# Kernel tuning notes

Measured on AMD Instinct MI355X. Metric: run time of the kernel, lower is better.

Reference implementation:

```python
import jax, jax.numpy as jnp
import numpy as np

N = 32768      # nodes
E = 524288     # edges (avg degree 16)
F = 64         # node_feat_dim
D = 64         # gnn_dim (= per-head out channels, concat=False)
ED = 32        # edge_feat_dim
L = 6          # num_layers
H = 2          # heads
C = D          # per-head channels
LN_EPS = 1e-5


def layer_norm(h, g, b):
    mu = jnp.mean(h, axis=-1, keepdims=True)
    var = jnp.mean((h - mu) ** 2, axis=-1, keepdims=True)
    return g * (h - mu) * jax.lax.rsqrt(var + LN_EPS) + b


def setup_inputs() -> dict:
    key = jax.random.key(0)
    ks = jax.random.split(key, 16)
    x = jax.random.normal(ks[0], (N, F), jnp.float32)
    edge_index = jax.random.randint(ks[1], (2, E), 0, N, jnp.int32)
    edge_attr = jax.random.normal(ks[2], (E, ED), jnp.float32)
    manual_gamma = 1.0 + 0.1 * jax.random.normal(ks[3], (L, D), jnp.float32)
    manual_beta = 0.1 * jax.random.normal(ks[4], (L, D), jnp.float32)
    # node_embed Linear(F, D)
    embed_W = jax.random.normal(ks[5], (F, D), jnp.float32) / np.float32(np.sqrt(F))
    embed_b = jnp.zeros((D,), jnp.float32)
    # per-layer LayerNorm affine params
    ln_gamma = jnp.ones((L, D), jnp.float32)
    ln_beta = jnp.zeros((L, D), jnp.float32)
    # per-layer GATConv params (shared lin for src/dst, PyG non-bipartite)
    lin_W = jax.random.normal(ks[6], (L, D, H * C), jnp.float32) / np.float32(np.sqrt(D))
    lin_edge_W = jax.random.normal(ks[7], (L, ED, H * C), jnp.float32) / np.float32(np.sqrt(ED))
    att_src = jax.random.normal(ks[8], (L, H, C), jnp.float32) / np.float32(np.sqrt(C))
    att_dst = jax.random.normal(ks[9], (L, H, C), jnp.float32) / np.float32(np.sqrt(C))
    att_edge = jax.random.normal(ks[10], (L, H, C), jnp.float32) / np.float32(np.sqrt(C))
    gat_bias = jnp.zeros((L, C), jnp.float32)
    # edge output head: Linear(2D+ED, D) -> ReLU -> Linear(D, 1)
    head_W1 = jax.random.normal(ks[11], (2 * D + ED, D), jnp.float32) / np.float32(np.sqrt(2 * D + ED))
    head_b1 = jnp.zeros((D,), jnp.float32)
    head_W2 = jax.random.normal(ks[12], (D, 1), jnp.float32) / np.float32(np.sqrt(D))
    head_b2 = jnp.zeros((1,), jnp.float32)
    return dict(x=x, edge_index=edge_index, edge_attr=edge_attr,
                manual_gamma=manual_gamma, manual_beta=manual_beta,
                embed_W=embed_W, embed_b=embed_b, ln_gamma=ln_gamma, ln_beta=ln_beta,
                lin_W=lin_W, lin_edge_W=lin_edge_W, att_src=att_src, att_dst=att_dst,
                att_edge=att_edge, gat_bias=gat_bias, head_W1=head_W1, head_b1=head_b1,
                head_W2=head_W2, head_b2=head_b2)


def reference(x, edge_index, edge_attr, manual_gamma, manual_beta,
              embed_W, embed_b, ln_gamma, ln_beta, lin_W, lin_edge_W,
              att_src, att_dst, att_edge, gat_bias, head_W1, head_b1,
              head_W2, head_b2):
    src, dst = edge_index[0], edge_index[1]
    # PyG GATConv default add_self_loops=True, fill_value='mean' for edge_attr
    loop = jnp.arange(N, dtype=edge_index.dtype)
    src_f = jnp.concatenate([src, loop])   # [E+N]
    dst_f = jnp.concatenate([dst, loop])
    deg = jax.ops.segment_sum(jnp.ones((E,), x.dtype), dst, num_segments=N)
    loop_attr = jax.ops.segment_sum(edge_attr, dst, num_segments=N) / jnp.maximum(deg, 1.0)[:, None]
    edge_attr_f = jnp.concatenate([edge_attr, loop_attr], axis=0)  # [E+N, ED]

    h = x @ embed_W + embed_b  # [N, D]
    for l in range(L):
        hn = layer_norm(h, ln_gamma[l], ln_beta[l])
        hm = manual_gamma[l][None, :] * hn + manual_beta[l][None, :]
        xh = (hm @ lin_W[l]).reshape(N, H, C)                      # [N,H,C]
        a_s = jnp.sum(xh * att_src[l][None], axis=-1)              # [N,H]
        a_d = jnp.sum(xh * att_dst[l][None], axis=-1)              # [N,H]
        eh = (edge_attr_f @ lin_edge_W[l]).reshape(-1, H, C)       # [E+N,H,C]
        a_e = jnp.sum(eh * att_edge[l][None], axis=-1)             # [E+N,H]
        alpha = jax.nn.leaky_relu(a_s[src_f] + a_d[dst_f] + a_e, 0.2)
        amax = jax.ops.segment_max(alpha, dst_f, num_segments=N)   # every node has a self-loop
        ex = jnp.exp(alpha - amax[dst_f])
        den = jax.ops.segment_sum(ex, dst_f, num_segments=N)
        w = ex / (den[dst_f] + 1e-16)                              # segment softmax [E+N,H]
        msg = xh[src_f] * w[..., None]                             # [E+N,H,C]
        out = jax.ops.segment_sum(msg, dst_f, num_segments=N)      # [N,H,C]
        h = jax.nn.relu(jnp.mean(out, axis=1) + gat_bias[l])       # concat=False -> head mean

    ef = jnp.concatenate([h[src], h[dst], edge_attr], axis=-1)     # [E, 2D+ED]
    hid = jax.nn.relu(ef @ head_W1 + head_b1)
    return (hid @ head_W2 + head_b2)[:, 0]                         # [E]
```

## Files before the change

### kernel.cpp

```cpp
#include <hip/hip_runtime.h>
#include <hip/hip_bf16.h>
#include <math.h>

#define NN 32768
#define EE 524288
#define LL 6

typedef __attribute__((ext_vector_type(8))) short short8;
typedef __attribute__((ext_vector_type(4))) float floatx4;
typedef __attribute__((ext_vector_type(4))) float fx4;
typedef __attribute__((ext_vector_type(4))) unsigned int ux4;

union U16x8 { short8 v; unsigned short u[8]; };

__device__ __forceinline__ unsigned short f2bf(float x) {
    union { float f; unsigned int u; } v; v.f = x;
    unsigned int r = v.u + 0x7fffu + ((v.u >> 16) & 1u);
    return (unsigned short)(r >> 16);
}
__device__ __forceinline__ float bf2f(unsigned short h) {
    union { unsigned int u; float f; } v; v.u = (unsigned int)h << 16;
    return v.f;
}


__global__ __launch_bounds__(1024) void scan_kernel(const int* __restrict__ deg,
                                                    int* __restrict__ row_ptr,
                                                    int* __restrict__ cnt) {
    __shared__ int bs[1024];
    int t = threadIdx.x;
    int base = t * 32;
    int loc[32];
    int s = 0;
#pragma unroll
    for (int i = 0; i < 32; ++i) { int v = deg[base + i]; loc[i] = s; s += v; }
    bs[t] = s;
    __syncthreads();
    for (int off = 1; off < 1024; off <<= 1) {
        int v = (t >= off) ? bs[t - off] : 0;
        __syncthreads();
        bs[t] += v;
        __syncthreads();
    }
    int pre = (t == 0) ? 0 : bs[t - 1];
#pragma unroll
    for (int i = 0; i < 32; ++i) { row_ptr[base + i] = pre + loc[i]; cnt[base + i] = 0; }
    if (t == 1023) row_ptr[NN] = bs[1023];
}

__global__ void fill_kernel(const int* __restrict__ src, const int* __restrict__ dst,
                            const float* __restrict__ aeo, const int* __restrict__ row_ptr,
                            int* __restrict__ cnt, float* __restrict__ aeP) {
    int e = blockIdx.x * 256 + threadIdx.x;
    if (e >= EE) return;
    int d = dst[e];
    int pos = row_ptr[d] + atomicAdd(&cnt[d], 1);
    const float2* ae2 = (const float2*)aeo;
    float2 a0 = ae2[e],          a1 = ae2[EE + e],     a2 = ae2[2 * EE + e];
    float2 a3 = ae2[3 * EE + e], a4 = ae2[4 * EE + e], a5 = ae2[5 * EE + e];
    fx4 r0 = {__int_as_float(src[e]), 0.f, a0.x, a0.y};
    fx4 r1 = {a1.x, a1.y, a2.x, a2.y};
    fx4 r2 = {a3.x, a3.y, a4.x, a4.y};
    fx4 r3 = {a5.x, a5.y, 0.f, 0.f};
    fx4* R = (fx4*)(aeP + (size_t)pos * 16);
    R[0] = r0; R[1] = r1; R[2] = r2; R[3] = r3;
}

__global__ __launch_bounds__(256) void smallprep_kernel(
    const float* __restrict__ lin_W, const float* __restrict__ head_W1,
    const float* __restrict__ lin_edge_W, const float* __restrict__ att_edge,
    const float* __restrict__ att_src, const float* __restrict__ att_dst,
    unsigned short* __restrict__ gBhi, unsigned short* __restrict__ gBlo,
    unsigned short* __restrict__ aeBhi, unsigned short* __restrict__ aeBlo,
    float* __restrict__ vs, float* __restrict__ vvd,
    unsigned short* __restrict__ w1chi, unsigned short* __restrict__ w1clo,
    int* __restrict__ deg) {
    __shared__ float svb[384];
    int bb = blockIdx.x;
    int tid = threadIdx.x;
    if (bb < 7) {
        unsigned short* dh = gBhi + (size_t)bb * 128 * 64;
        unsigned short* dl = gBlo + (size_t)bb * 128 * 64;
        if (bb < 6) {
            int n2 = tid & 63, kh = tid >> 6;
            U16x8 hh[4], ll[4];
            for (int kk = 0; kk < 32; ++kk) {
                int j = kh * 32 + kk;
                int h = j >> 6, k = j & 63;
                float wv = 0.5f * lin_W[((size_t)bb * 64 + k) * 128 + h * 64 + n2];
                unsigned short h16 = f2bf(wv);
                hh[kk >> 3].u[kk & 7] = h16;
                ll[kk >> 3].u[kk & 7] = f2bf(wv - bf2f(h16));
            }
#pragma unroll
            for (int c = 0; c < 4; ++c) {
                int cg = kh * 4 + c;
                int off = n2 * 128 + ((cg ^ (n2 & 15)) << 3);
                *(short8*)(dh + off) = hh[c].v;
                *(short8*)(dl + off) = ll[c].v;
            }
        } else {
            int n = tid & 127, kh = tid >> 7;
            U16x8 hh[4], ll[4];
            for (int kk = 0; kk < 32; ++kk) {
                int k = kh * 32 + kk;
                float wv = (n < 64) ? head_W1[k * 64 + n] : head_W1[(64 + k) * 64 + (n - 64)];
                unsigned short h16 = f2bf(wv);
                hh[kk >> 3].u[kk & 7] = h16;
                ll[kk >> 3].u[kk & 7] = f2bf(wv - bf2f(h16));
            }
#pragma unroll
            for (int c = 0; c < 4; ++c) {
                int cg = kh * 4 + c;
                int off = n * 64 + ((cg ^ (n & 7)) << 3);
                *(short8*)(dh + off) = hh[c].v;
                *(short8*)(dl + off) = ll[c].v;
            }
        }
    } else if (bb == 7) {
        for (int t = tid; t < 384; t += 256) {
            int l = t / 64; int r = t & 63; int ed = r >> 1; int hh = r & 1;
            const float* w = lin_edge_W + l * 32 * 128 + ed * 128 + hh * 64;
            const float* a = att_edge + l * 128 + hh * 64;
            float s = 0.f;
#pragma unroll 8
            for (int c = 0; c < 64; ++c) s += w[c] * a[c];
            svb[t] = s;
        }
        int n = tid & 63, kc = tid >> 6;
#pragma unroll
        for (int j = 0; j < 8; ++j) {
            int k = kc * 8 + j;
            float wv = head_W1[(128 + k) * 64 + n];
            unsigned short h16 = f2bf(wv);
            w1chi[n * 32 + k] = h16;
            w1clo[n * 32 + k] = f2bf(wv - bf2f(h16));
        }
        __syncthreads();
        if (tid < 64) {
            int n2 = tid & 15, q = tid >> 4;
            U16x8 hi, lo;
#pragma unroll
            for (int i = 0; i < 8; ++i) {
                int k = q * 8 + i;
                float val = (n2 < 12) ? svb[(n2 >> 1) * 64 + k * 2 + (n2 & 1)] : 0.f;
                unsigned short h16 = f2bf(val);
                hi.u[i] = h16;
                lo.u[i] = f2bf(val - bf2f(h16));
            }
            *(short8*)(aeBhi + tid * 8) = hi.v;
            *(short8*)(aeBlo + tid * 8) = lo.v;
        }
    } else if (bb < 14) {
        int l = bb - 8;
        int sel = tid >> 7, idx = tid & 127;
        int h = idx >> 6, k = idx & 63;
        const float* att = (sel ? att_dst : att_src) + l * 128 + h * 64;
        const float* wr = lin_W + ((size_t)l * 64 + k) * 128 + h * 64;
        float s = 0.f;
#pragma unroll 8
        for (int c = 0; c < 64; ++c) s += wr[c] * att[c];
        (sel ? vvd : vs)[l * 128 + idx] = s;
    } else {
        int i = (bb - 14) * 1024 + tid * 4;
        *(int4*)(deg + i) = make_int4(0, 0, 0, 0);
    }
}

__global__ __launch_bounds__(256) void ae_deg_kernel(
    const float* __restrict__ edge_attr, const int* __restrict__ dst,
    const unsigned short* __restrict__ aeBhi, const unsigned short* __restrict__ aeBlo,
    float* __restrict__ aeo, unsigned short* __restrict__ eabf, int* __restrict__ deg) {
    __shared__ float tr[4][64 * 13];
    int tid = threadIdx.x;
    int w = tid >> 6, lane = tid & 63;
    int e0 = blockIdx.x * 256 + w * 64;
    int e = blockIdx.x * 256 + tid;
    atomicAdd(&deg[dst[e]], 1);
    short8 bhi = *(const short8*)(aeBhi + lane * 8);
    short8 blo = *(const short8*)(aeBlo + lane * 8);
    int r = lane & 15, q = lane >> 4;
    float* trw = tr[w];
#pragma unroll
    for (int t = 0; t < 4; ++t) {
        int er = e0 + t * 16 + r;
        const fx4* p = (const fx4*)(edge_attr + (size_t)er * 32 + q * 8);
        fx4 f0 = __builtin_nontemporal_load(p);
        fx4 f1 = __builtin_nontemporal_load(p + 1);
        float av[8] = {f0.x, f0.y, f0.z, f0.w, f1.x, f1.y, f1.z, f1.w};
        U16x8 hi, lo;
#pragma unroll
        for (int jj = 0; jj < 8; ++jj) {
            unsigned short h16 = f2bf(av[jj]);
            hi.u[jj] = h16;
            lo.u[jj] = f2bf(av[jj] - bf2f(h16));
        }
        __builtin_nontemporal_store(hi.v, (short8*)(eabf + (size_t)er * 32 + q * 8));
        floatx4 acc = {};
        acc = __builtin_amdgcn_mfma_f32_16x16x32_bf16(lo.v, bhi, acc, 0, 0, 0);
        acc = __builtin_amdgcn_mfma_f32_16x16x32_bf16(hi.v, blo, acc, 0, 0, 0);
        acc = __builtin_amdgcn_mfma_f32_16x16x32_bf16(hi.v, bhi, acc, 0, 0, 0);
        if (r < 12) {
#pragma unroll
            for (int rr = 0; rr < 4; ++rr)
                trw[(t * 16 + q * 4 + rr) * 13 + r] = acc[rr];
        }
    }
#pragma unroll
    for (int l = 0; l < LL; ++l) {
        float2 v2;
        v2.x = trw[lane * 13 + l * 2];
        v2.y = trw[lane * 13 + l * 2 + 1];
        *(float2*)(aeo + (size_t)l * EE * 2 + (size_t)(e0 + lane) * 2) = v2;
    }
}

__global__ __launch_bounds__(256) void embed_ln_kernel(
    const float* __restrict__ x, const float* __restrict__ W, const float* __restrict__ b,
    const float* __restrict__ ln_g, const float* __restrict__ ln_b,
    const float* __restrict__ mg, const float* __restrict__ mb,
    const float* __restrict__ vs0, const float* __restrict__ vd0,
    unsigned short* __restrict__ hm_bf, float* __restrict__ a_s, float* __restrict__ a_d) {
    __shared__ float xr[4][64];
    int w = threadIdx.x >> 6, j = threadIdx.x & 63;
    int n = blockIdx.x * 4 + w;
    xr[w][j] = x[(size_t)n * 64 + j];
    __syncthreads();
    float acc = b[j];
#pragma unroll 8
    for (int k = 0; k < 64; ++k) acc += xr[w][k] * W[k * 64 + j];
    float s = acc, sq = acc * acc;
    for (int off = 1; off < 64; off <<= 1) { s += __shfl_xor(s, off); sq += __shfl_xor(sq, off); }
    float mu = s * (1.f / 64.f);
    float var = sq * (1.f / 64.f) - mu * mu;
    float rs = rsqrtf(var + 1e-5f);
    float hm = mg[j] * (ln_g[j] * (acc - mu) * rs + ln_b[j]) + mb[j];
    hm_bf[(size_t)n * 64 + j] = f2bf(hm);
    float s0 = hm * vs0[j], s1 = hm * vs0[64 + j];
    float d0 = hm * vd0[j], d1 = hm * vd0[64 + j];
    for (int off = 1; off < 64; off <<= 1) {
        s0 += __shfl_xor(s0, off); s1 += __shfl_xor(s1, off);
        d0 += __shfl_xor(d0, off); d1 += __shfl_xor(d1, off);
    }
    if (j == 0) {
        a_s[n * 2] = s0; a_s[n * 2 + 1] = s1;
        a_d[n * 2] = d0; a_d[n * 2 + 1] = d1;
    }
}

__device__ __forceinline__ void fma8h(uint4 pv, float w, float* a) {
    unsigned int u[4] = {pv.x, pv.y, pv.z, pv.w};
#pragma unroll
    for (int q = 0; q < 4; ++q) {
        union { unsigned int x; float f; } lo, hi;
        lo.x = u[q] << 16; hi.x = u[q] & 0xffff0000u;
        a[2 * q]     += w * lo.f;
        a[2 * q + 1] += w * hi.f;
    }
}

__global__ __launch_bounds__(256) void aggregate10_kernel(
    const unsigned short* __restrict__ hm_bf, const float* __restrict__ a_s,
    const float* __restrict__ a_d, const float* __restrict__ aeP,
    const int* __restrict__ row_ptr, unsigned short* __restrict__ Abf, int aeoff) {
    __shared__ float stg[4][4][64][4];
    int w = threadIdx.x >> 6, lane = threadIdx.x & 63;
    int g = lane >> 4, j = lane & 15;
    int ch = j & 7, hh = j >> 3;
    int n = blockIdx.x * 16 + w * 4 + g;
    const float2* as2 = (const float2*)a_s;
    const uint4* hmv = (const uint4*)hm_bf;
    float2 adn = ((const float2*)a_d)[n];
    float2 asn = as2[n];
    uint4 pvself = hmv[(size_t)n * 8 + ch];
    int beg = row_ptr[n], end = row_ptr[n + 1];
    int degn = end - beg;

    float acc[8] = {};
    float den = 0.f, aex = 0.f, aey = 0.f;
    float* sg = &stg[w][g][0][0];

    for (int base = 0; base < degn; base += 64) {
        int cnt = degn - base; cnt = cnt > 64 ? 64 : cnt;
        int nchunk = (cnt + 15) >> 4;
        for (int it = 0; it < nchunk; ++it) {
            int s0 = it * 16;
            int rem = cnt - s0;
            float w0v = 0.f, w1v = 0.f;
            int sval = 0;
            if (j < rem) {
                const char* rec = (const char*)aeP + ((size_t)(beg + base + s0 + j) << 6);
                int sv = *(const int*)rec;
                float2 ae = *(const float2*)(rec + aeoff);
                float2 as = as2[sv];
                aex += ae.x; aey += ae.y;
                float al0 = as.x + adn.x + ae.x; al0 = al0 > 0.f ? al0 : 0.2f * al0;
                float al1 = as.y + adn.y + ae.y; al1 = al1 > 0.f ? al1 : 0.2f * al1;
                w0v = __expf(al0);
                w1v = __expf(al1);
                sval = sv;
            }
            float4 st;
            st.x = __int_as_float(sval); st.y = w0v; st.z = w1v; st.w = 0.f;
            *(float4*)(sg + (s0 + j) * 4) = st;
        }
        int c8 = (cnt + 7) & ~7;
        for (int s = 0; s < c8; s += 8) {
            float4 m[8];
#pragma unroll
            for (int u = 0; u < 8; ++u) m[u] = *(const float4*)(sg + (s + u) * 4);
            uint4 p[8];
#pragma unroll
            for (int u = 0; u < 8; ++u) p[u] = hmv[(size_t)__float_as_int(m[u].x) * 8 + ch];
#pragma unroll
            for (int u = 0; u < 8; ++u) {
                float b = hh ? m[u].z : m[u].y;
                den += b;
                fma8h(p[u], b, acc);
            }
        }
    }
#pragma unroll
    for (int m = 1; m < 16; m <<= 1) {
        aex += __shfl_xor(aex, m);
        aey += __shfl_xor(aey, m);
    }
    float invd = 1.f / fmaxf((float)degn, 1.f);
    float al0 = asn.x + adn.x + aex * invd; al0 = al0 > 0.f ? al0 : 0.2f * al0;
    float al1 = asn.y + adn.y + aey * invd; al1 = al1 > 0.f ? al1 : 0.2f * al1;
    float ws = hh ? __expf(al1) : __expf(al0);
    den += ws;
    fma8h(pvself, ws, acc);
    float inv = 1.f / (den + 1e-16f);
    U16x8 hb;
#pragma unroll
    for (int q = 0; q < 8; ++q) hb.u[q] = f2bf(acc[q] * inv);
    int cg = hh * 8 + ch;
    __builtin_nontemporal_store(hb.v, (short8*)(Abf + (size_t)n * 128 + ((cg ^ (n & 15)) << 3)));
}

__global__ __launch_bounds__(256) void post_gemm(
    const unsigned short* __restrict__ Abf, const unsigned short* __restrict__ gBhi,
    const unsigned short* __restrict__ gBlo, const float* __restrict__ bias,
    const float* __restrict__ ln_g, const float* __restrict__ ln_b,
    const float* __restrict__ mg, const float* __restrict__ mb,
    const float* __restrict__ vsn, const float* __restrict__ vdn,
    unsigned short* __restrict__ hm_bf, float* __restrict__ a_s, float* __restrict__ a_d) {
    __shared__ unsigned short Ahi[64 * 128];
    __shared__ unsigned short Bhi[64 * 128], Blo[64 * 128];
    int tid = threadIdx.x;
    {
        const ux4* sa = (const ux4*)(Abf + (size_t)blockIdx.x * 64 * 128);
        const uint4* sh = (const uint4*)gBhi;
        const uint4* sl = (const uint4*)gBlo;
        for (int i = tid; i < 1024; i += 256) {
            ((ux4*)Ahi)[i] = __builtin_nontemporal_load(sa + i);
            ((uint4*)Bhi)[i] = sh[i];
            ((uint4*)Blo)[i] = sl[i];
        }
    }
    __syncthreads();

    int w = tid >> 6, lane = tid & 63, col = lane & 15, quad = lane >> 4;
    int m = w * 16 + col;
    floatx4 acc[4] = {};
#pragma unroll
    for (int s = 0; s < 4; ++s) {
        int ca = (quad + 4 * s) ^ col;
        short8 ahi = *(const short8*)(Ahi + m * 128 + ca * 8);
#pragma unroll
        for (int t = 0; t < 4; ++t) {
            int off = (t * 16 + col) * 128 + ca * 8;
            short8 bhi = *(const short8*)(Bhi + off);
            short8 blo = *(const short8*)(Blo + off);
            acc[t] = __builtin_amdgcn_mfma_f32_16x16x32_bf16(ahi, blo, acc[t], 0, 0, 0);
            acc[t] = __builtin_amdgcn_mfma_f32_16x16x32_bf16(ahi, bhi, acc[t], 0, 0, 0);
        }
    }
    int nodebase = blockIdx.x * 64 + w * 16;
    float bv[4];
#pragma unroll
    for (int t = 0; t < 4; ++t) bv[t] = bias[t * 16 + col];
    float vsv[4], vsv1[4], vdv[4], vdv1[4], lg[4], lb[4], mgv[4], mbv[4];
#pragma unroll
    for (int t = 0; t < 4; ++t) {
        int c = t * 16 + col;
        vsv[t] = vsn[c]; vsv1[t] = vsn[64 + c];
        vdv[t] = vdn[c]; vdv1[t] = vdn[64 + c];
        lg[t] = ln_g[c]; lb[t] = ln_b[c];
        mgv[t] = mg[c]; mbv[t] = mb[c];
    }
#pragma unroll
    for (int r = 0; r < 4; ++r) {
        int node = nodebase + quad * 4 + r;
        float hv[4];
        float s = 0.f, sq = 0.f;
#pragma unroll
        for (int t = 0; t < 4; ++t) {
            float v = acc[t][r] + bv[t];
            v = v > 0.f ? v : 0.f;
            hv[t] = v;
            s += v; sq += v * v;
        }
        for (int off = 1; off < 16; off <<= 1) { s += __shfl_xor(s, off); sq += __shfl_xor(sq, off); }
        float mu = s * (1.f / 64.f);
        float var = sq * (1.f / 64.f) - mu * mu;
        float rs = rsqrtf(var + 1e-5f);
        float s0 = 0.f, s1 = 0.f, d0 = 0.f, d1 = 0.f;
#pragma unroll
        for (int t = 0; t < 4; ++t) {
            float hmv = mgv[t] * (lg[t] * (hv[t] - mu) * rs + lb[t]) + mbv[t];
            hm_bf[(size_t)node * 64 + t * 16 + col] = f2bf(hmv);
            s0 += hmv * vsv[t]; s1 += hmv * vsv1[t];
            d0 += hmv * vdv[t]; d1 += hmv * vdv1[t];
        }
        for (int off = 1; off < 16; off <<= 1) {
            s0 += __shfl_xor(s0, off); s1 += __shfl_xor(s1, off);
            d0 += __shfl_xor(d0, off); d1 += __shfl_xor(d1, off);
        }
        if (col == 0) {
            a_s[node * 2] = s0; a_s[node * 2 + 1] = s1;
            a_d[node * 2] = d0; a_d[node * 2 + 1] = d1;
        }
    }
}

__global__ __launch_bounds__(256) void postuv_gemm(
    const unsigned short* __restrict__ Abf, const unsigned short* __restrict__ gB5hi,
    const unsigned short* __restrict__ gB5lo, const float* __restrict__ bias,
    const unsigned short* __restrict__ gB6hi, const unsigned short* __restrict__ gB6lo,
    unsigned short* __restrict__ uv) {
    __shared__ unsigned short lds[24576];
    unsigned short* Ahi  = lds;
    unsigned short* B5hi = lds + 8192;
    unsigned short* B5lo = lds + 16384;
    unsigned short* A2hi = lds;
    unsigned short* A2lo = lds + 4096;
    unsigned short* B6hi = lds + 8192;
    unsigned short* B6lo = lds + 16384;
    int tid = threadIdx.x;
    {
        const ux4* sa = (const ux4*)(Abf + (size_t)blockIdx.x * 64 * 128);
        const uint4* sh = (const uint4*)gB5hi;
        const uint4* sl = (const uint4*)gB5lo;
        for (int i = tid; i < 1024; i += 256) {
            ((ux4*)Ahi)[i] = __builtin_nontemporal_load(sa + i);
            ((uint4*)B5hi)[i] = sh[i];
            ((uint4*)B5lo)[i] = sl[i];
        }
    }
    __syncthreads();

    int w = tid >> 6, lane = tid & 63, col = lane & 15, quad = lane >> 4;
    int m = w * 16 + col;
    floatx4 acc[4] = {};
#pragma unroll
    for (int s = 0; s < 4; ++s) {
        int ca = (quad + 4 * s) ^ col;
        short8 ahi = *(const short8*)(Ahi + m * 128 + ca * 8);
#pragma unroll
        for (int t = 0; t < 4; ++t) {
            int off = (t * 16 + col) * 128 + ca * 8;
            short8 bhi = *(const short8*)(B5hi + off);
            short8 blo = *(const short8*)(B5lo + off);
            acc[t] = __builtin_amdgcn_mfma_f32_16x16x32_bf16(ahi, blo, acc[t], 0, 0, 0);
            acc[t] = __builtin_amdgcn_mfma_f32_16x16x32_bf16(ahi, bhi, acc[t], 0, 0, 0);
        }
    }
    float bv[4];
#pragma unroll
    for (int t = 0; t < 4; ++t) bv[t] = bias[t * 16 + col];
    __syncthreads();
#pragma unroll
    for (int t = 0; t < 4; ++t) {
        int c = t * 16 + col;
        int cg = c >> 3, cr = c & 7;
#pragma unroll
        for (int r = 0; r < 4; ++r) {
            float v = acc[t][r] + bv[t];
            v = v > 0.f ? v : 0.f;
            int i = w * 16 + quad * 4 + r;
            int off = i * 64 + ((cg ^ (i & 7)) << 3) + cr;
            unsigned short hh = f2bf(v);
            A2hi[off] = hh;
            A2lo[off] = f2bf(v - bf2f(hh));
        }
    }
    for (int i = tid; i < 1024; i += 256) {
        ((uint4*)B6hi)[i] = ((const uint4*)gB6hi)[i];
        ((uint4*)B6lo)[i] = ((const uint4*)gB6lo)[i];
    }
    __syncthreads();

    floatx4 acc2[8] = {};
#pragma unroll
    for (int s = 0; s < 2; ++s) {
        int ca = (quad + 4 * s) ^ (col & 7);
        short8 a2h = *(const short8*)(A2hi + m * 64 + ca * 8);
        short8 a2l = *(const short8*)(A2lo + m * 64 + ca * 8);
#pragma unroll
        for (int t = 0; t < 8; ++t) {
            int off = (t * 16 + col) * 64 + ca * 8;
            short8 bh = *(const short8*)(B6hi + off);
            short8 bl = *(const short8*)(B6lo + off);
            acc2[t] = __builtin_amdgcn_mfma_f32_16x16x32_bf16(a2l, bh, acc2[t], 0, 0, 0);
            acc2[t] = __builtin_amdgcn_mfma_f32_16x16x32_bf16(a2h, bl, acc2[t], 0, 0, 0);
            acc2[t] = __builtin_amdgcn_mfma_f32_16x16x32_bf16(a2h, bh, acc2[t], 0, 0, 0);
        }
    }
    int nodebase = blockIdx.x * 64 + w * 16;
#pragma unroll
    for (int t = 0; t < 8; ++t)
#pragma unroll
        for (int r = 0; r < 4; ++r)
            uv[(size_t)(nodebase + quad * 4 + r) * 128 + t * 16 + col] = f2bf(acc2[t][r]);
}

__global__ __launch_bounds__(256) void head2_kernel(
    const unsigned short* __restrict__ uv, const int* __restrict__ src,
    const int* __restrict__ dst, const unsigned short* __restrict__ eabf,
    const unsigned short* __restrict__ w1chi, const unsigned short* __restrict__ w1clo,
    const float* __restrict__ b1, const float* __restrict__ W2,
    const float* __restrict__ b2, float* __restrict__ out) {
    __shared__ float g[64][68];
    __shared__ unsigned short Abf[64 * 40];
    __shared__ unsigned short Bh[64 * 40], Bl[64 * 40];
    __shared__ int sA[64], dA[64];
    int tid = threadIdx.x;
    int base = blockIdx.x * 64;
    if (tid < 64) sA[tid] = src[base + tid];
    else if (tid < 128) dA[tid - 64] = dst[base + tid - 64];
    {
        int n = tid >> 2, c = tid & 3;
        *(short8*)(Bh + n * 40 + c * 8) = *(const short8*)(w1chi + n * 32 + c * 8);
        *(short8*)(Bl + n * 40 + c * 8) = *(const short8*)(w1clo + n * 32 + c * 8);
    }
    {
        int e = tid >> 2, q = tid & 3;
        short8 v = __builtin_nontemporal_load(
            (const short8*)(eabf + (size_t)(base + e) * 32 + q * 8));
        *(short8*)(Abf + e * 40 + q * 8) = v;
    }
    __syncthreads();
    {
        int e = tid >> 2, q = tid & 3;
        const uint4* su = (const uint4*)(uv + (size_t)sA[e] * 128);
        const uint4* dv = (const uint4*)(uv + (size_t)dA[e] * 128);
        uint4 U0 = su[2 * q], U1 = su[2 * q + 1];
        uint4 V0 = dv[8 + 2 * q], V1 = dv[9 + 2 * q];
        const float4* b1p = (const float4*)(b1 + q * 16);
        float bb[16];
#pragma unroll
        for (int j = 0; j < 4; ++j) {
            float4 b4 = b1p[j];
            bb[4 * j] = b4.x; bb[4 * j + 1] = b4.y; bb[4 * j + 2] = b4.z; bb[4 * j + 3] = b4.w;
        }
        unsigned int uw[8] = {U0.x, U0.y, U0.z, U0.w, U1.x, U1.y, U1.z, U1.w};
        unsigned int vw[8] = {V0.x, V0.y, V0.z, V0.w, V1.x, V1.y, V1.z, V1.w};
        float* gr = &g[e][q * 16];
#pragma unroll
        for (int j = 0; j < 8; ++j) {
            gr[2 * j] = bf2f((unsigned short)(uw[j] & 0xffff)) +
                        bf2f((unsigned short)(vw[j] & 0xffff)) + bb[2 * j];
            gr[2 * j + 1] = bf2f((unsigned short)(uw[j] >> 16)) +
                            bf2f((unsigned short)(vw[j] >> 16)) + bb[2 * j + 1];
        }
    }
    __syncthreads();

    int lane = tid & 63, w = tid >> 6, col = lane & 15, quad = lane >> 4;
    short8 a = *(const short8*)(Abf + (w * 16 + col) * 40 + quad * 8);
    floatx4 acc[4] = {};
#pragma unroll
    for (int t = 0; t < 4; ++t) {
        int off = (t * 16 + col) * 40 + quad * 8;
        short8 bh = *(const short8*)(Bh + off);
        short8 bl = *(const short8*)(Bl + off);
        acc[t] = __builtin_amdgcn_mfma_f32_16x16x32_bf16(a, bl, acc[t], 0, 0, 0);
        acc[t] = __builtin_amdgcn_mfma_f32_16x16x32_bf16(a, bh, acc[t], 0, 0, 0);
    }
    float sv[4] = {0.f, 0.f, 0.f, 0.f};
#pragma unroll
    for (int t = 0; t < 4; ++t) {
        float w2v = W2[t * 16 + col];
#pragma unroll
        for (int r = 0; r < 4; ++r) {
            float hid = acc[t][r] + g[w * 16 + quad * 4 + r][t * 16 + col];
            hid = hid > 0.f ? hid : 0.f;
            sv[r] += hid * w2v;
        }
    }
    float b2v = b2[0];
#pragma unroll
    for (int r = 0; r < 4; ++r) {
        float v = sv[r];
        v += __shfl_xor(v, 1);
        v += __shfl_xor(v, 2);
        v += __shfl_xor(v, 4);
        v += __shfl_xor(v, 8);
        if (col == 0) out[base + w * 16 + quad * 4 + r] = v + b2v;
    }
}


extern "C" void kernel_launch(void* const* d_in, const int* in_sizes, int n_in,
                              void* d_out, int out_size, void* d_ws, size_t ws_size,
                              hipStream_t stream) {
    const float* x            = (const float*)d_in[0];
    const int*   edge_index   = (const int*)d_in[1];
    const float* edge_attr    = (const float*)d_in[2];
    const float* manual_gamma = (const float*)d_in[3];
    const float* manual_beta  = (const float*)d_in[4];
    const float* embed_W      = (const float*)d_in[5];
    const float* embed_b      = (const float*)d_in[6];
    const float* ln_gamma     = (const float*)d_in[7];
    const float* ln_beta      = (const float*)d_in[8];
    const float* lin_W        = (const float*)d_in[9];
    const float* lin_edge_W   = (const float*)d_in[10];
    const float* att_src      = (const float*)d_in[11];
    const float* att_dst      = (const float*)d_in[12];
    const float* att_edge     = (const float*)d_in[13];
    const float* gat_bias     = (const float*)d_in[14];
    const float* head_W1      = (const float*)d_in[15];
    const float* head_b1      = (const float*)d_in[16];
    const float* head_W2      = (const float*)d_in[17];
    const float* head_b2      = (const float*)d_in[18];
    float* out = (float*)d_out;

    const int* src = edge_index;
    const int* dst = edge_index + EE;

    char* ws = (char*)d_ws;
    size_t off = 0;
    auto alloc = [&](size_t bytes) {
        void* p = ws + off;
        off += (bytes + 255) & ~(size_t)255;
        return p;
    };
    int*   deg        = (int*)alloc(NN * 4);
    int*   row_ptr    = (int*)alloc((NN + 1) * 4);
    int*   cnt        = (int*)alloc(NN * 4);
    float* aeP        = (float*)alloc((size_t)EE * 64);
    float* aeo        = (float*)alloc((size_t)LL * EE * 2 * 4);
    float* vs         = (float*)alloc(LL * 128 * 4);
    float* vvd        = (float*)alloc(LL * 128 * 4);
    float* a_s        = (float*)alloc((size_t)NN * 2 * 4);
    float* a_d        = (float*)alloc((size_t)NN * 2 * 4);
    unsigned short* Abf   = (unsigned short*)alloc((size_t)NN * 128 * 2);
    unsigned short* hm_bf = (unsigned short*)alloc((size_t)NN * 64 * 2);
    unsigned short* uvbuf = (unsigned short*)alloc((size_t)NN * 128 * 2);
    unsigned short* eabf  = (unsigned short*)alloc((size_t)EE * 32 * 2);
    unsigned short* gBhi  = (unsigned short*)alloc((size_t)7 * 128 * 64 * 2);
    unsigned short* gBlo  = (unsigned short*)alloc((size_t)7 * 128 * 64 * 2);
    unsigned short* w1chi = (unsigned short*)alloc(64 * 32 * 2);
    unsigned short* w1clo = (unsigned short*)alloc(64 * 32 * 2);
    unsigned short* aeBhi = (unsigned short*)alloc(64 * 8 * 2);
    unsigned short* aeBlo = (unsigned short*)alloc(64 * 8 * 2);
    if (off > ws_size) return;

    smallprep_kernel<<<46, 256, 0, stream>>>(lin_W, head_W1, lin_edge_W, att_edge,
                                             att_src, att_dst, gBhi, gBlo, aeBhi, aeBlo,
                                             vs, vvd, w1chi, w1clo, deg);
    ae_deg_kernel<<<EE / 256, 256, 0, stream>>>(edge_attr, dst, aeBhi, aeBlo, aeo, eabf, deg);
    scan_kernel<<<1, 1024, 0, stream>>>(deg, row_ptr, cnt);
    fill_kernel<<<EE / 256, 256, 0, stream>>>(src, dst, aeo, row_ptr, cnt, aeP);
    embed_ln_kernel<<<NN / 4, 256, 0, stream>>>(x, embed_W, embed_b, ln_gamma, ln_beta,
                                                manual_gamma, manual_beta, vs, vvd,
                                                hm_bf, a_s, a_d);

    for (int l = 0; l < LL; ++l) {
        aggregate10_kernel<<<NN / 16, 256, 0, stream>>>(
            hm_bf, a_s, a_d, aeP, row_ptr, Abf, 8 + 8 * l);
        if (l < LL - 1) {
            post_gemm<<<NN / 64, 256, 0, stream>>>(
                Abf, gBhi + (size_t)l * 128 * 64, gBlo + (size_t)l * 128 * 64,
                gat_bias + l * 64, ln_gamma + (l + 1) * 64, ln_beta + (l + 1) * 64,
                manual_gamma + (l + 1) * 64, manual_beta + (l + 1) * 64,
                vs + (l + 1) * 128, vvd + (l + 1) * 128, hm_bf, a_s, a_d);
        } else {
            postuv_gemm<<<NN / 64, 256, 0, stream>>>(
                Abf, gBhi + (size_t)l * 128 * 64, gBlo + (size_t)l * 128 * 64,
                gat_bias + l * 64, gBhi + (size_t)6 * 128 * 64,
                gBlo + (size_t)6 * 128 * 64, uvbuf);
        }
    }

    head2_kernel<<<EE / 64, 256, 0, stream>>>(uvbuf, src, dst, eabf, w1chi, w1clo,
                                              head_b1, head_W2, head_b2, out);
}
```

Before: 456.5 us.

## Fuse aggregation into post-GEMM kernels and compute edge logits in CSR order

Folds the per-layer attention aggregation into the following GEMM/LayerNorm kernel, so the aggregated bf16 tile stays in LDS and no longer goes through a global Abf buffer. Node features and attention scalars are ping-ponged between two buffers, because fused blocks now read the previous layer's state while other blocks write the new one. Edge-attention logits are computed after CSR sorting, one compact per-layer 16-byte record per edge instead of a 64-byte packed record. The head kernel now converts edge_attr to bf16 on the fly instead of reading a precomputed buffer. In exchange, only 512 fused blocks each aggregate 64 nodes serially, which may cut parallelism and latency hiding, and the edge_attr reads in CSR order are scattered.

```diff
diff --git a/kernel.cpp b/kernel.cpp
--- a/kernel.cpp
+++ b/kernel.cpp
@@ -9,7 +9,6 @@
 typedef __attribute__((ext_vector_type(8))) short short8;
 typedef __attribute__((ext_vector_type(4))) float floatx4;
 typedef __attribute__((ext_vector_type(4))) float fx4;
-typedef __attribute__((ext_vector_type(4))) unsigned int ux4;
 
 union U16x8 { short8 v; unsigned short u[8]; };
 
@@ -23,6 +22,15 @@
     return v.f;
 }
 
+
+__global__ void deg_kernel(const int* __restrict__ dst, int* __restrict__ deg) {
+    int i = (blockIdx.x * 256 + threadIdx.x) * 4;
+    int4 d = *(const int4*)(dst + i);
+    atomicAdd(&deg[d.x], 1);
+    atomicAdd(&deg[d.y], 1);
+    atomicAdd(&deg[d.z], 1);
+    atomicAdd(&deg[d.w], 1);
+}
 
 __global__ __launch_bounds__(1024) void scan_kernel(const int* __restrict__ deg,
                                                     int* __restrict__ row_ptr,
@@ -49,21 +57,13 @@
 }
 
 __global__ void fill_kernel(const int* __restrict__ src, const int* __restrict__ dst,
-                            const float* __restrict__ aeo, const int* __restrict__ row_ptr,
-                            int* __restrict__ cnt, float* __restrict__ aeP) {
+                            const int* __restrict__ row_ptr, int* __restrict__ cnt,
+                            int2* __restrict__ sedge) {
     int e = blockIdx.x * 256 + threadIdx.x;
     if (e >= EE) return;
     int d = dst[e];
     int pos = row_ptr[d] + atomicAdd(&cnt[d], 1);
-    const float2* ae2 = (const float2*)aeo;
-    float2 a0 = ae2[e],          a1 = ae2[EE + e],     a2 = ae2[2 * EE + e];
-    float2 a3 = ae2[3 * EE + e], a4 = ae2[4 * EE + e], a5 = ae2[5 * EE + e];
-    fx4 r0 = {__int_as_float(src[e]), 0.f, a0.x, a0.y};
-    fx4 r1 = {a1.x, a1.y, a2.x, a2.y};
-    fx4 r2 = {a3.x, a3.y, a4.x, a4.y};
-    fx4 r3 = {a5.x, a5.y, 0.f, 0.f};
-    fx4* R = (fx4*)(aeP + (size_t)pos * 16);
-    R[0] = r0; R[1] = r1; R[2] = r2; R[3] = r3;
+    sedge[pos] = make_int2(e, src[e]);
 }
 
 __global__ __launch_bounds__(256) void smallprep_kernel(
@@ -167,26 +167,23 @@
     }
 }
 
-__global__ __launch_bounds__(256) void ae_deg_kernel(
-    const float* __restrict__ edge_attr, const int* __restrict__ dst,
+__global__ __launch_bounds__(256) void ae_csr_kernel(
+    const float* __restrict__ edge_attr, const int2* __restrict__ sedge,
     const unsigned short* __restrict__ aeBhi, const unsigned short* __restrict__ aeBlo,
-    float* __restrict__ aeo, unsigned short* __restrict__ eabf, int* __restrict__ deg) {
+    float* __restrict__ aeL) {
     __shared__ float tr[4][64 * 13];
     int tid = threadIdx.x;
     int w = tid >> 6, lane = tid & 63;
-    int e0 = blockIdx.x * 256 + w * 64;
-    int e = blockIdx.x * 256 + tid;
-    atomicAdd(&deg[dst[e]], 1);
+    int p0 = blockIdx.x * 256 + w * 64;
     short8 bhi = *(const short8*)(aeBhi + lane * 8);
     short8 blo = *(const short8*)(aeBlo + lane * 8);
     int r = lane & 15, q = lane >> 4;
     float* trw = tr[w];
 #pragma unroll
     for (int t = 0; t < 4; ++t) {
-        int er = e0 + t * 16 + r;
-        const fx4* p = (const fx4*)(edge_attr + (size_t)er * 32 + q * 8);
-        fx4 f0 = __builtin_nontemporal_load(p);
-        fx4 f1 = __builtin_nontemporal_load(p + 1);
+        int eg = sedge[p0 + t * 16 + r].x;
+        const fx4* p = (const fx4*)(edge_attr + (size_t)eg * 32 + q * 8);
+        fx4 f0 = p[0], f1 = p[1];
         float av[8] = {f0.x, f0.y, f0.z, f0.w, f1.x, f1.y, f1.z, f1.w};
         U16x8 hi, lo;
 #pragma unroll
@@ -195,7 +192,6 @@
             hi.u[jj] = h16;
             lo.u[jj] = f2bf(av[jj] - bf2f(h16));
         }
-        __builtin_nontemporal_store(hi.v, (short8*)(eabf + (size_t)er * 32 + q * 8));
         floatx4 acc = {};
         acc = __builtin_amdgcn_mfma_f32_16x16x32_bf16(lo.v, bhi, acc, 0, 0, 0);
         acc = __builtin_amdgcn_mfma_f32_16x16x32_bf16(hi.v, blo, acc, 0, 0, 0);
@@ -206,12 +202,15 @@
                 trw[(t * 16 + q * 4 + rr) * 13 + r] = acc[rr];
         }
     }
+    int2 sl = sedge[p0 + lane];
 #pragma unroll
     for (int l = 0; l < LL; ++l) {
-        float2 v2;
-        v2.x = trw[lane * 13 + l * 2];
-        v2.y = trw[lane * 13 + l * 2 + 1];
-        *(float2*)(aeo + (size_t)l * EE * 2 + (size_t)(e0 + lane) * 2) = v2;
+        fx4 rec;
+        rec.x = __int_as_float(sl.y);
+        rec.y = trw[lane * 13 + l * 2];
+        rec.z = trw[lane * 13 + l * 2 + 1];
+        rec.w = 0.f;
+        __builtin_nontemporal_store(rec, (fx4*)(aeL + ((size_t)l * EE + p0 + lane) * 4));
     }
 }
 
@@ -259,27 +258,16 @@
     }
 }
 
-__global__ __launch_bounds__(256) void aggregate10_kernel(
-    const unsigned short* __restrict__ hm_bf, const float* __restrict__ a_s,
-    const float* __restrict__ a_d, const float* __restrict__ aeP,
-    const int* __restrict__ row_ptr, unsigned short* __restrict__ Abf, int aeoff) {
-    __shared__ float stg[4][4][64][4];
-    int w = threadIdx.x >> 6, lane = threadIdx.x & 63;
-    int g = lane >> 4, j = lane & 15;
-    int ch = j & 7, hh = j >> 3;
-    int n = blockIdx.x * 16 + w * 4 + g;
-    const float2* as2 = (const float2*)a_s;
-    const uint4* hmv = (const uint4*)hm_bf;
-    float2 adn = ((const float2*)a_d)[n];
+__device__ __forceinline__ void agg_node(
+    int n, int ch, int hh, int j, const uint4* hmv, const float2* as2,
+    const float* ad_in, const float* aeLl, const int* row_ptr, float* sg, U16x8& hb) {
+    float2 adn = ((const float2*)ad_in)[n];
     float2 asn = as2[n];
     uint4 pvself = hmv[(size_t)n * 8 + ch];
     int beg = row_ptr[n], end = row_ptr[n + 1];
     int degn = end - beg;
-
     float acc[8] = {};
     float den = 0.f, aex = 0.f, aey = 0.f;
-    float* sg = &stg[w][g][0][0];
-
     for (int base = 0; base < degn; base += 64) {
         int cnt = degn - base; cnt = cnt > 64 ? 64 : cnt;
         int nchunk = (cnt + 15) >> 4;
@@ -289,13 +277,12 @@
             float w0v = 0.f, w1v = 0.f;
             int sval = 0;
             if (j < rem) {
-                const char* rec = (const char*)aeP + ((size_t)(beg + base + s0 + j) << 6);
-                int sv = *(const int*)rec;
-                float2 ae = *(const float2*)(rec + aeoff);
+                fx4 rv = *(const fx4*)(aeLl + ((size_t)(beg + base + s0 + j)) * 4);
+                int sv = __float_as_int(rv.x);
                 float2 as = as2[sv];
-                aex += ae.x; aey += ae.y;
-                float al0 = as.x + adn.x + ae.x; al0 = al0 > 0.f ? al0 : 0.2f * al0;
-                float al1 = as.y + adn.y + ae.y; al1 = al1 > 0.f ? al1 : 0.2f * al1;
+                aex += rv.y; aey += rv.z;
+                float al0 = as.x + adn.x + rv.y; al0 = al0 > 0.f ? al0 : 0.2f * al0;
+                float al1 = as.y + adn.y + rv.z; al1 = al1 > 0.f ? al1 : 0.2f * al1;
                 w0v = __expf(al0);
                 w1v = __expf(al1);
                 sval = sv;
@@ -332,36 +319,53 @@
     den += ws;
     fma8h(pvself, ws, acc);
     float inv = 1.f / (den + 1e-16f);
-    U16x8 hb;
 #pragma unroll
     for (int q = 0; q < 8; ++q) hb.u[q] = f2bf(acc[q] * inv);
-    int cg = hh * 8 + ch;
-    __builtin_nontemporal_store(hb.v, (short8*)(Abf + (size_t)n * 128 + ((cg ^ (n & 15)) << 3)));
-}
-
-__global__ __launch_bounds__(256) void post_gemm(
-    const unsigned short* __restrict__ Abf, const unsigned short* __restrict__ gBhi,
-    const unsigned short* __restrict__ gBlo, const float* __restrict__ bias,
-    const float* __restrict__ ln_g, const float* __restrict__ ln_b,
-    const float* __restrict__ mg, const float* __restrict__ mb,
-    const float* __restrict__ vsn, const float* __restrict__ vdn,
-    unsigned short* __restrict__ hm_bf, float* __restrict__ a_s, float* __restrict__ a_d) {
-    __shared__ unsigned short Ahi[64 * 128];
-    __shared__ unsigned short Bhi[64 * 128], Blo[64 * 128];
+}
+
+__global__ __launch_bounds__(256) void fused_post(
+    const unsigned short* __restrict__ hm_in, const float* __restrict__ as_in,
+    const float* __restrict__ ad_in, const float* __restrict__ aeLl,
+    const int* __restrict__ row_ptr,
+    const unsigned short* __restrict__ gBhi, const unsigned short* __restrict__ gBlo,
+    const float* __restrict__ bias, const float* __restrict__ ln_g,
+    const float* __restrict__ ln_b, const float* __restrict__ mg,
+    const float* __restrict__ mb, const float* __restrict__ vsn,
+    const float* __restrict__ vdn, unsigned short* __restrict__ hm_out,
+    float* __restrict__ as_out, float* __restrict__ ad_out) {
+    __shared__ char smem[49152];
+    unsigned short* Ahi = (unsigned short*)smem;
+    float* stgAll = (float*)(smem + 16384);
+    unsigned short* Bhi = (unsigned short*)(smem + 16384);
+    unsigned short* Blo = (unsigned short*)(smem + 32768);
     int tid = threadIdx.x;
+    int w = tid >> 6, lane = tid & 63;
+    int g = lane >> 4, j = lane & 15;
+    int ch = j & 7, hh = j >> 3;
+    const float2* as2 = (const float2*)as_in;
+    const uint4* hmv = (const uint4*)hm_in;
+    float* sg = stgAll + w * 1024 + g * 256;
+    int nb = blockIdx.x * 64;
+
+    for (int rr = 0; rr < 4; ++rr) {
+        int m = w * 16 + rr * 4 + g;
+        U16x8 hb;
+        agg_node(nb + m, ch, hh, j, hmv, as2, ad_in, aeLl, row_ptr, sg, hb);
+        int cg = hh * 8 + ch;
+        *(short8*)(Ahi + m * 128 + ((cg ^ (m & 15)) << 3)) = hb.v;
+    }
+    __syncthreads();
     {
-        const ux4* sa = (const ux4*)(Abf + (size_t)blockIdx.x * 64 * 128);
         const uint4* sh = (const uint4*)gBhi;
         const uint4* sl = (const uint4*)gBlo;
         for (int i = tid; i < 1024; i += 256) {
-            ((ux4*)Ahi)[i] = __builtin_nontemporal_load(sa + i);
             ((uint4*)Bhi)[i] = sh[i];
             ((uint4*)Blo)[i] = sl[i];
         }
     }
     __syncthreads();
 
-    int w = tid >> 6, lane = tid & 63, col = lane & 15, quad = lane >> 4;
+    int col = lane & 15, quad = lane >> 4;
     int m = w * 16 + col;
     floatx4 acc[4] = {};
 #pragma unroll
@@ -377,7 +381,7 @@
             acc[t] = __builtin_amdgcn_mfma_f32_16x16x32_bf16(ahi, bhi, acc[t], 0, 0, 0);
         }
     }
-    int nodebase = blockIdx.x * 64 + w * 16;
+    int nodebase = nb + w * 16;
     float bv[4];
 #pragma unroll
     for (int t = 0; t < 4; ++t) bv[t] = bias[t * 16 + col];
@@ -409,49 +413,67 @@
         float s0 = 0.f, s1 = 0.f, d0 = 0.f, d1 = 0.f;
 #pragma unroll
         for (int t = 0; t < 4; ++t) {
-            float hmv = mgv[t] * (lg[t] * (hv[t] - mu) * rs + lb[t]) + mbv[t];
-            hm_bf[(size_t)node * 64 + t * 16 + col] = f2bf(hmv);
-            s0 += hmv * vsv[t]; s1 += hmv * vsv1[t];
-            d0 += hmv * vdv[t]; d1 += hmv * vdv1[t];
+            float hmval = mgv[t] * (lg[t] * (hv[t] - mu) * rs + lb[t]) + mbv[t];
+            hm_out[(size_t)node * 64 + t * 16 + col] = f2bf(hmval);
+            s0 += hmval * vsv[t]; s1 += hmval * vsv1[t];
+            d0 += hmval * vdv[t]; d1 += hmval * vdv1[t];
         }
         for (int off = 1; off < 16; off <<= 1) {
             s0 += __shfl_xor(s0, off); s1 += __shfl_xor(s1, off);
             d0 += __shfl_xor(d0, off); d1 += __shfl_xor(d1, off);
         }
         if (col == 0) {
-            a_s[node * 2] = s0; a_s[node * 2 + 1] = s1;
-            a_d[node * 2] = d0; a_d[node * 2 + 1] = d1;
-        }
-    }
-}
-
-__global__ __launch_bounds__(256) void postuv_gemm(
-    const unsigned short* __restrict__ Abf, const unsigned short* __restrict__ gB5hi,
-    const unsigned short* __restrict__ gB5lo, const float* __restrict__ bias,
+            as_out[node * 2] = s0; as_out[node * 2 + 1] = s1;
+            ad_out[node * 2] = d0; ad_out[node * 2 + 1] = d1;
+        }
+    }
+}
+
+__global__ __launch_bounds__(256) void fused_uv(
+    const unsigned short* __restrict__ hm_in, const float* __restrict__ as_in,
+    const float* __restrict__ ad_in, const float* __restrict__ aeLl,
+    const int* __restrict__ row_ptr,
+    const unsigned short* __restrict__ gB5hi, const unsigned short* __restrict__ gB5lo,
+    const float* __restrict__ bias,
     const unsigned short* __restrict__ gB6hi, const unsigned short* __restrict__ gB6lo,
     unsigned short* __restrict__ uv) {
-    __shared__ unsigned short lds[24576];
-    unsigned short* Ahi  = lds;
-    unsigned short* B5hi = lds + 8192;
-    unsigned short* B5lo = lds + 16384;
-    unsigned short* A2hi = lds;
-    unsigned short* A2lo = lds + 4096;
-    unsigned short* B6hi = lds + 8192;
-    unsigned short* B6lo = lds + 16384;
+    __shared__ char smem[49152];
+    unsigned short* Ahi  = (unsigned short*)smem;
+    float* stgAll        = (float*)(smem + 16384);
+    unsigned short* B5hi = (unsigned short*)(smem + 16384);
+    unsigned short* B5lo = (unsigned short*)(smem + 32768);
+    unsigned short* A2hi = (unsigned short*)smem;
+    unsigned short* A2lo = (unsigned short*)(smem + 8192);
+    unsigned short* B6hi = (unsigned short*)(smem + 16384);
+    unsigned short* B6lo = (unsigned short*)(smem + 32768);
     int tid = threadIdx.x;
+    int w = tid >> 6, lane = tid & 63;
+    int g = lane >> 4, j = lane & 15;
+    int ch = j & 7, hh = j >> 3;
+    const float2* as2 = (const float2*)as_in;
+    const uint4* hmv = (const uint4*)hm_in;
+    float* sg = stgAll + w * 1024 + g * 256;
+    int nb = blockIdx.x * 64;
+
+    for (int rr = 0; rr < 4; ++rr) {
+        int m = w * 16 + rr * 4 + g;
+        U16x8 hb;
+        agg_node(nb + m, ch, hh, j, hmv, as2, ad_in, aeLl, row_ptr, sg, hb);
+        int cg = hh * 8 + ch;
+        *(short8*)(Ahi + m * 128 + ((cg ^ (m & 15)) << 3)) = hb.v;
+    }
+    __syncthreads();
     {
-        const ux4* sa = (const ux4*)(Abf + (size_t)blockIdx.x * 64 * 128);
         const uint4* sh = (const uint4*)gB5hi;
         const uint4* sl = (const uint4*)gB5lo;
         for (int i = tid; i < 1024; i += 256) {
-            ((ux4*)Ahi)[i] = __builtin_nontemporal_load(sa + i);
             ((uint4*)B5hi)[i] = sh[i];
             ((uint4*)B5lo)[i] = sl[i];
         }
     }
     __syncthreads();
 
-    int w = tid >> 6, lane = tid & 63, col = lane & 15, quad = lane >> 4;
+    int col = lane & 15, quad = lane >> 4;
     int m = w * 16 + col;
     floatx4 acc[4] = {};
 #pragma unroll
@@ -481,9 +503,9 @@
             v = v > 0.f ? v : 0.f;
             int i = w * 16 + quad * 4 + r;
             int off = i * 64 + ((cg ^ (i & 7)) << 3) + cr;
-            unsigned short hh = f2bf(v);
-            A2hi[off] = hh;
-            A2lo[off] = f2bf(v - bf2f(hh));
+            unsigned short hhv = f2bf(v);
+            A2hi[off] = hhv;
+            A2lo[off] = f2bf(v - bf2f(hhv));
         }
     }
     for (int i = tid; i < 1024; i += 256) {
@@ -508,7 +530,7 @@
             acc2[t] = __builtin_amdgcn_mfma_f32_16x16x32_bf16(a2h, bh, acc2[t], 0, 0, 0);
         }
     }
-    int nodebase = blockIdx.x * 64 + w * 16;
+    int nodebase = nb + w * 16;
 #pragma unroll
     for (int t = 0; t < 8; ++t)
 #pragma unroll
@@ -518,7 +540,7 @@
 
 __global__ __launch_bounds__(256) void head2_kernel(
     const unsigned short* __restrict__ uv, const int* __restrict__ src,
-    const int* __restrict__ dst, const unsigned short* __restrict__ eabf,
+    const int* __restrict__ dst, const float* __restrict__ edge_attr,
     const unsigned short* __restrict__ w1chi, const unsigned short* __restrict__ w1clo,
     const float* __restrict__ b1, const float* __restrict__ W2,
     const float* __restrict__ b2, float* __restrict__ out) {
@@ -537,9 +559,14 @@
     }
     {
         int e = tid >> 2, q = tid & 3;
-        short8 v = __builtin_nontemporal_load(
-            (const short8*)(eabf + (size_t)(base + e) * 32 + q * 8));
-        *(short8*)(Abf + e * 40 + q * 8) = v;
+        const fx4* p = (const fx4*)(edge_attr + (size_t)(base + e) * 32 + q * 8);
+        fx4 f0 = __builtin_nontemporal_load(p);
+        fx4 f1 = __builtin_nontemporal_load(p + 1);
+        float av[8] = {f0.x, f0.y, f0.z, f0.w, f1.x, f1.y, f1.z, f1.w};
+        U16x8 cv;
+#pragma unroll
+        for (int jj = 0; jj < 8; ++jj) cv.u[jj] = f2bf(av[jj]);
+        *(short8*)(Abf + e * 40 + q * 8) = cv.v;
     }
     __syncthreads();
     {
@@ -551,19 +578,19 @@
         const float4* b1p = (const float4*)(b1 + q * 16);
         float bb[16];
 #pragma unroll
-        for (int j = 0; j < 4; ++j) {
-            float4 b4 = b1p[j];
-            bb[4 * j] = b4.x; bb[4 * j + 1] = b4.y; bb[4 * j + 2] = b4.z; bb[4 * j + 3] = b4.w;
+        for (int jj = 0; jj < 4; ++jj) {
+            float4 b4 = b1p[jj];
+            bb[4 * jj] = b4.x; bb[4 * jj + 1] = b4.y; bb[4 * jj + 2] = b4.z; bb[4 * jj + 3] = b4.w;
         }
         unsigned int uw[8] = {U0.x, U0.y, U0.z, U0.w, U1.x, U1.y, U1.z, U1.w};
         unsigned int vw[8] = {V0.x, V0.y, V0.z, V0.w, V1.x, V1.y, V1.z, V1.w};
         float* gr = &g[e][q * 16];
 #pragma unroll
-        for (int j = 0; j < 8; ++j) {
-            gr[2 * j] = bf2f((unsigned short)(uw[j] & 0xffff)) +
-                        bf2f((unsigned short)(vw[j] & 0xffff)) + bb[2 * j];
-            gr[2 * j + 1] = bf2f((unsigned short)(uw[j] >> 16)) +
-                            bf2f((unsigned short)(vw[j] >> 16)) + bb[2 * j + 1];
+        for (int jj = 0; jj < 8; ++jj) {
+            gr[2 * jj] = bf2f((unsigned short)(uw[jj] & 0xffff)) +
+                         bf2f((unsigned short)(vw[jj] & 0xffff)) + bb[2 * jj];
+            gr[2 * jj + 1] = bf2f((unsigned short)(uw[jj] >> 16)) +
+                             bf2f((unsigned short)(vw[jj] >> 16)) + bb[2 * jj + 1];
         }
     }
     __syncthreads();
@@ -640,16 +667,17 @@
     int*   deg        = (int*)alloc(NN * 4);
     int*   row_ptr    = (int*)alloc((NN + 1) * 4);
     int*   cnt        = (int*)alloc(NN * 4);
-    float* aeP        = (float*)alloc((size_t)EE * 64);
-    float* aeo        = (float*)alloc((size_t)LL * EE * 2 * 4);
+    int2*  sedge      = (int2*)alloc((size_t)EE * 8);
+    float* aeL        = (float*)alloc((size_t)LL * EE * 16);
     float* vs         = (float*)alloc(LL * 128 * 4);
     float* vvd        = (float*)alloc(LL * 128 * 4);
-    float* a_s        = (float*)alloc((size_t)NN * 2 * 4);
-    float* a_d        = (float*)alloc((size_t)NN * 2 * 4);
-    unsigned short* Abf   = (unsigned short*)alloc((size_t)NN * 128 * 2);
-    unsigned short* hm_bf = (unsigned short*)alloc((size_t)NN * 64 * 2);
+    float* asA        = (float*)alloc((size_t)NN * 2 * 4);
+    float* asB        = (float*)alloc((size_t)NN * 2 * 4);
+    float* adA        = (float*)alloc((size_t)NN * 2 * 4);
+    float* adB        = (float*)alloc((size_t)NN * 2 * 4);
+    unsigned short* hmA   = (unsigned short*)alloc((size_t)NN * 64 * 2);
+    unsigned short* hmB   = (unsigned short*)alloc((size_t)NN * 64 * 2);
     unsigned short* uvbuf = (unsigned short*)alloc((size_t)NN * 128 * 2);
-    unsigned short* eabf  = (unsigned short*)alloc((size_t)EE * 32 * 2);
     unsigned short* gBhi  = (unsigned short*)alloc((size_t)7 * 128 * 64 * 2);
     unsigned short* gBlo  = (unsigned short*)alloc((size_t)7 * 128 * 64 * 2);
     unsigned short* w1chi = (unsigned short*)alloc(64 * 32 * 2);
@@ -661,30 +689,38 @@
     smallprep_kernel<<<46, 256, 0, stream>>>(lin_W, head_W1, lin_edge_W, att_edge,
                                              att_src, att_dst, gBhi, gBlo, aeBhi, aeBlo,
                                              vs, vvd, w1chi, w1clo, deg);
-    ae_deg_kernel<<<EE / 256, 256, 0, stream>>>(edge_attr, dst, aeBhi, aeBlo, aeo, eabf, deg);
+    deg_kernel<<<EE / 1024, 256, 0, stream>>>(dst, deg);
     scan_kernel<<<1, 1024, 0, stream>>>(deg, row_ptr, cnt);
-    fill_kernel<<<EE / 256, 256, 0, stream>>>(src, dst, aeo, row_ptr, cnt, aeP);
+    fill_kernel<<<EE / 256, 256, 0, stream>>>(src, dst, row_ptr, cnt, sedge);
+    ae_csr_kernel<<<EE / 256, 256, 0, stream>>>(edge_attr, sedge, aeBhi, aeBlo, aeL);
     embed_ln_kernel<<<NN / 4, 256, 0, stream>>>(x, embed_W, embed_b, ln_gamma, ln_beta,
                                                 manual_gamma, manual_beta, vs, vvd,
-                                                hm_bf, a_s, a_d);
+                                                hmA, asA, adA);
 
     for (int l = 0; l < LL; ++l) {
-        aggregate10_kernel<<<NN / 16, 256, 0, stream>>>(
-            hm_bf, a_s, a_d, aeP, row_ptr, Abf, 8 + 8 * l);
+        const unsigned short* hin = (l & 1) ? hmB : hmA;
+        unsigned short* hout = (l & 1) ? hmA : hmB;
+        const float* asi = (l & 1) ? asB : asA;
+        float* aso = (l & 1) ? asA : asB;
+        const float* adi = (l & 1) ? adB : adA;
+        float* ado = (l & 1) ? adA : adB;
+        const float* aeLl = aeL + (size_t)l * EE * 4;
         if (l < LL - 1) {
-            post_gemm<<<NN / 64, 256, 0, stream>>>(
-                Abf, gBhi + (size_t)l * 128 * 64, gBlo + (size_t)l * 128 * 64,
+            fused_post<<<NN / 64, 256, 0, stream>>>(
+                hin, asi, adi, aeLl, row_ptr,
+                gBhi + (size_t)l * 128 * 64, gBlo + (size_t)l * 128 * 64,
                 gat_bias + l * 64, ln_gamma + (l + 1) * 64, ln_beta + (l + 1) * 64,
                 manual_gamma + (l + 1) * 64, manual_beta + (l + 1) * 64,
-                vs + (l + 1) * 128, vvd + (l + 1) * 128, hm_bf, a_s, a_d);
+                vs + (l + 1) * 128, vvd + (l + 1) * 128, hout, aso, ado);
         } else {
-            postuv_gemm<<<NN / 64, 256, 0, stream>>>(
-                Abf, gBhi + (size_t)l * 128 * 64, gBlo + (size_t)l * 128 * 64,
+            fused_uv<<<NN / 64, 256, 0, stream>>>(
+                hin, asi, adi, aeLl, row_ptr,
+                gBhi + (size_t)l * 128 * 64, gBlo + (size_t)l * 128 * 64,
                 gat_bias + l * 64, gBhi + (size_t)6 * 128 * 64,
                 gBlo + (size_t)6 * 128 * 64, uvbuf);
         }
     }
 
-    head2_kernel<<<EE / 64, 256, 0, stream>>>(uvbuf, src, dst, eabf, w1chi, w1clo,
+    head2_kernel<<<EE / 64, 256, 0, stream>>>(uvbuf, src, dst, edge_attr, w1chi, w1clo,
                                               head_b1, head_W2, head_b2, out);
 }
```

After: 444.1 us. 1.03x faster.
